# Optimization experiments

Measured on AMD Instinct MI355X. Metric: run time of the kernel, lower is better.

The kernel has to match this reference:

```python
import jax, jax.numpy as jnp
import numpy as np

EPS = 1e-6
NUM_HEADS = 16
ROPE_THETA = 100000.0


def _rope_tables(seq_len, head_dim, theta):
    inv_freq = 1.0 / (theta ** (np.arange(0, head_dim, 2, dtype=np.float32) / head_dim))
    t = np.arange(seq_len, dtype=np.float32)
    freqs = np.outer(t, inv_freq)                      # (S, head_dim//2)
    emb = np.concatenate([freqs, freqs], axis=-1)      # (S, head_dim)
    return jnp.asarray(np.cos(emb))[None], jnp.asarray(np.sin(emb))[None]  # (1,S,D)


def setup_inputs() -> dict:
    key = jax.random.key(0)
    ks = jax.random.split(key, 6)
    B, S, H = 2, 2048, 1024
    head_dim = H // NUM_HEADS
    cos, sin = _rope_tables(S, head_dim, ROPE_THETA)
    scale = 0.02
    return {
        "hidden_states": jax.random.normal(ks[0], (B, S, H), dtype=jnp.float32),
        "cos": cos, "sin": sin,
        "Wq": jax.random.normal(ks[1], (H, H), dtype=jnp.float32) * scale,
        "bq": jnp.zeros((H,), dtype=jnp.float32),
        "Wk": jax.random.normal(ks[2], (H, H), dtype=jnp.float32) * scale,
        "bk": jnp.zeros((H,), dtype=jnp.float32),
        "Wv": jax.random.normal(ks[3], (H, H), dtype=jnp.float32) * scale,
        "bv": jnp.zeros((H,), dtype=jnp.float32),
        "Wo": jax.random.normal(ks[4], (H, H), dtype=jnp.float32) * scale,
        "bo": jnp.zeros((H,), dtype=jnp.float32),
        "rms_weight": jnp.ones((H,), dtype=jnp.float32),
    }


def _rms_norm(x, w):
    var = jnp.mean(x * x, axis=-1, keepdims=True)
    return x * jax.lax.rsqrt(var + EPS) * w


def _rotate_half(x):
    x1, x2 = jnp.split(x, 2, axis=-1)
    return jnp.concatenate([-x2, x1], axis=-1)


def reference(hidden_states, cos, sin, Wq, bq, Wk, bk, Wv, bv, Wo, bo, rms_weight):
    B, S, H = hidden_states.shape
    D = H // NUM_HEADS
    q = hidden_states @ Wq.T + bq
    k = hidden_states @ Wk.T + bk
    v = hidden_states @ Wv.T + bv
    # RMSNorm over full hidden dim BEFORE head split (as in original)
    q = _rms_norm(q, rms_weight)
    k = _rms_norm(k, rms_weight)
    # (B,S,H) -> (B,heads,S,D)
    q = q.reshape(B, S, NUM_HEADS, D).transpose(0, 2, 1, 3)
    k = k.reshape(B, S, NUM_HEADS, D).transpose(0, 2, 1, 3)
    v = v.reshape(B, S, NUM_HEADS, D).transpose(0, 2, 1, 3)
    # RoPE: cos/sin (1,S,D) -> unsqueeze head dim
    c = cos[:, None, :, :]
    s = sin[:, None, :, :]
    q = q * c + _rotate_half(q) * s
    k = k * c + _rotate_half(k) * s
    # attention (faithful: boolean tril mask is ADDED as 0/1, not -inf)
    scale = D ** 0.5
    scores = jnp.einsum("bhqd,bhkd->bhqk", q, k) / scale
    mask = jnp.tril(jnp.ones((S, S), dtype=scores.dtype))  # +1 on causal, +0 elsewhere
    attn = jax.nn.softmax(scores + mask, axis=-1)
    out = jnp.einsum("bhqk,bhkd->bhqd", attn, v)
    out = out.transpose(0, 2, 1, 3).reshape(B, S, H)
    return out @ Wo.T + bo
```

## Files before the change

kernel.cpp:

```cpp
#include <hip/hip_runtime.h>

typedef unsigned short u16;
typedef __attribute__((ext_vector_type(8))) short bf16x8;
typedef __attribute__((ext_vector_type(4))) float f32x4;

#define MFMA16(A,B,C) __builtin_amdgcn_mfma_f32_16x16x32_bf16(A,B,C,0,0,0)
#define LOG2E 1.4426950408889634f
#define C1 0.18033688011112042f

__device__ __forceinline__ u16 f2bf(float f){
  unsigned int u; __builtin_memcpy(&u,&f,4);
  unsigned int r = (u + 0x7fffu + ((u>>16)&1u)) >> 16;
  return (u16)r;
}
__device__ __forceinline__ float bf2f(u16 h){
  unsigned int u = ((unsigned int)h) << 16;
  float f; __builtin_memcpy(&f,&u,4); return f;
}
__device__ __forceinline__ unsigned int pack_bf16(float a, float b){
  unsigned int ua, ub;
  __builtin_memcpy(&ua,&a,4); __builtin_memcpy(&ub,&b,4);
  ua = ua + 0x7fffu + ((ua>>16)&1u);
  ub = ub + 0x7fffu + ((ub>>16)&1u);
  return __builtin_amdgcn_perm(ub, ua, 0x07060302);
}

__device__ __forceinline__ void async_ld16(const void* g, void* l) {
  __builtin_amdgcn_global_load_lds(
      (const __attribute__((address_space(1))) unsigned int*)g,
      (__attribute__((address_space(3))) unsigned int*)l, 16, 0, 0);
}

__global__ __launch_bounds__(256) void cast_all(const float* __restrict__ hs,
    const float* __restrict__ wq, const float* __restrict__ wk,
    const float* __restrict__ wv, const float* __restrict__ wo,
    u16* __restrict__ dst)
{
  unsigned int i = blockIdx.x*256 + threadIdx.x;
  size_t el = (size_t)i * 8;
  const float* src; size_t off;
  if (el < 4194304) { src = hs; off = el; }
  else {
    unsigned int r = (unsigned int)((el - 4194304) >> 20);
    src = (r==0)?wq:(r==1)?wk:(r==2)?wv:wo;
    off = (el - 4194304) & 1048575;
  }
  float4 a = *reinterpret_cast<const float4*>(src+off);
  float4 b = *reinterpret_cast<const float4*>(src+off+4);
  u16 tmp[8] = {f2bf(a.x),f2bf(a.y),f2bf(a.z),f2bf(a.w),
                f2bf(b.x),f2bf(b.y),f2bf(b.z),f2bf(b.w)};
  *reinterpret_cast<uint4*>(dst + el) = *reinterpret_cast<const uint4*>(tmp);
}

__global__ __launch_bounds__(256) void gemm_qkv(const u16* __restrict__ A,
                                                const u16* __restrict__ W,
                                                const float* __restrict__ b0p,
                                                const float* __restrict__ b1p,
                                                const float* __restrict__ b2p,
                                                u16* __restrict__ out,
                                                int M, int N, int K)
{
  __shared__ __align__(16) u16 lds_a[128*32];
  __shared__ __align__(16) u16 lds_w[128*32];
  const int t = threadIdx.x;
  const int lane = t & 63, wave = t >> 6;
  const int wm = wave >> 1, wn = wave & 1;
  const int lr = lane & 15, quad = lane >> 4;
  const int n0 = blockIdx.x * 128, m0 = blockIdx.y * 128;
  const int wbase = t & 192;

  const f32x4 fzero = {0.f,0.f,0.f,0.f};
  f32x4 acc[4][4];
  #pragma unroll
  for (int i=0;i<4;++i)
    #pragma unroll
    for (int j=0;j<4;++j) acc[i][j] = fzero;

  for (int k0 = 0; k0 < K; k0 += 32) {
    __syncthreads();
    #pragma unroll
    for (int it=0; it<2; ++it) {
      int idx = it*256 + t;
      int row = idx >> 2, c8 = (idx & 3) * 8;
      int lbase = (it*256 + wbase) * 8;
      async_ld16(&A[(size_t)(m0+row)*K + k0 + c8], &lds_a[lbase]);
      async_ld16(&W[(size_t)(n0+row)*K + k0 + c8], &lds_w[lbase]);
    }
    __syncthreads();
    bf16x8 af[4], bfr[4];
    #pragma unroll
    for (int mt=0; mt<4; ++mt)
      af[mt] = *reinterpret_cast<const bf16x8*>(&lds_a[(wm*64 + mt*16 + lr)*32 + quad*8]);
    #pragma unroll
    for (int nt=0; nt<4; ++nt)
      bfr[nt] = *reinterpret_cast<const bf16x8*>(&lds_w[(wn*64 + nt*16 + lr)*32 + quad*8]);
    #pragma unroll
    for (int mt=0; mt<4; ++mt)
      #pragma unroll
      for (int nt=0; nt<4; ++nt)
        acc[mt][nt] = MFMA16(af[mt], bfr[nt], acc[mt][nt]);
  }

  int which = n0 >> 10;
  const float* bp = (which==0) ? b0p : (which==1) ? b1p : b2p;
  u16* dst = out + (size_t)which * 4194304;
  if (which == 2) {
    #pragma unroll
    for (int nt=0; nt<4; ++nt) {
      int nn = (n0 & 1023) + wn*64 + nt*16 + lr;
      float bv = bp[nn];
      int hh = nn >> 6, d = nn & 63;
      #pragma unroll
      for (int mt=0; mt<4; ++mt) {
        int m = m0 + wm*64 + mt*16 + quad*4;
        int b = m >> 11, s = m & 2047;
        u16 o[4];
        #pragma unroll
        for (int r=0; r<4; ++r) o[r] = f2bf(acc[mt][nt][r] + bv);
        *reinterpret_cast<uint2*>(&dst[((size_t)(b*16 + hh)*64 + d)*2048 + s]) =
            *reinterpret_cast<const uint2*>(o);
      }
    }
  } else {
    #pragma unroll
    for (int nt=0; nt<4; ++nt) {
      int nn = (n0 & 1023) + wn*64 + nt*16 + lr;
      float bv = bp[nn];
      int hh = nn >> 6, d = nn & 63;
      #pragma unroll
      for (int mt=0; mt<4; ++mt)
        #pragma unroll
        for (int r=0; r<4; ++r) {
          int m = m0 + wm*64 + mt*16 + quad*4 + r;
          int b = m >> 11, s = m & 2047;
          dst[((size_t)(b*16 + hh) * 2048 + s) * 64 + d] = f2bf(acc[mt][nt][r] + bv);
        }
    }
  }
}

__global__ __launch_bounds__(256) void gemm_o(const u16* __restrict__ A,
                                              const u16* __restrict__ W,
                                              const float* __restrict__ bias,
                                              float* __restrict__ O,
                                              int M, int N, int K)
{
  __shared__ __align__(16) u16 lds_a[128*32];
  __shared__ __align__(16) u16 lds_w[64*32];
  const int t = threadIdx.x;
  const int lane = t & 63, wm = t >> 6;
  const int lr = lane & 15, quad = lane >> 4;
  const int n0 = blockIdx.x * 64, m0 = blockIdx.y * 128;
  const int wbase = t & 192;

  const f32x4 fzero = {0.f,0.f,0.f,0.f};
  f32x4 acc[2][4];
  #pragma unroll
  for (int i=0;i<2;++i)
    #pragma unroll
    for (int j=0;j<4;++j) acc[i][j] = fzero;

  for (int k0 = 0; k0 < K; k0 += 32) {
    __syncthreads();
    #pragma unroll
    for (int it=0; it<2; ++it) {
      int idx = it*256 + t;
      int row = idx >> 2, c8 = (idx & 3) * 8;
      int lbase = (it*256 + wbase) * 8;
      async_ld16(&A[(size_t)(m0+row)*K + k0 + c8], &lds_a[lbase]);
    }
    async_ld16(&W[(size_t)(n0 + (t>>2))*K + k0 + (t&3)*8], &lds_w[wbase*8]);
    __syncthreads();
    bf16x8 af[2], bfr[4];
    #pragma unroll
    for (int mt=0; mt<2; ++mt)
      af[mt] = *reinterpret_cast<const bf16x8*>(&lds_a[(wm*32 + mt*16 + lr)*32 + quad*8]);
    #pragma unroll
    for (int nt=0; nt<4; ++nt)
      bfr[nt] = *reinterpret_cast<const bf16x8*>(&lds_w[(nt*16 + lr)*32 + quad*8]);
    #pragma unroll
    for (int mt=0; mt<2; ++mt)
      #pragma unroll
      for (int nt=0; nt<4; ++nt)
        acc[mt][nt] = MFMA16(af[mt], bfr[nt], acc[mt][nt]);
  }

  #pragma unroll
  for (int nt=0; nt<4; ++nt) {
    int n = n0 + nt*16 + lr;
    float bv = bias[n];
    #pragma unroll
    for (int mt=0; mt<2; ++mt)
      #pragma unroll
      for (int r=0; r<4; ++r) {
        int m = m0 + wm*32 + mt*16 + quad*4 + r;
        O[(size_t)m * N + n] = acc[mt][nt][r] + bv;
      }
  }
}

__global__ __launch_bounds__(256) void rmsrope(u16* __restrict__ qb, u16* __restrict__ kb,
                                               const float* __restrict__ cosb,
                                               const float* __restrict__ sinb,
                                               const float* __restrict__ w)
{
  u16* buf = blockIdx.y ? kb : qb;
  const int bs = blockIdx.x;
  const int b = bs >> 11, s = bs & 2047;
  const int t = threadIdx.x;
  float x1[2], x2[2];
  float ss = 0.f;
  #pragma unroll
  for (int i=0;i<2;++i){
    int p = t + i*256;
    int h = p >> 5, d = p & 31;
    size_t base = ((size_t)(b*16+h)*2048 + s)*64;
    x1[i] = bf2f(buf[base + d]);
    x2[i] = bf2f(buf[base + d + 32]);
    ss += x1[i]*x1[i] + x2[i]*x2[i];
  }
  #pragma unroll
  for (int off=32; off>0; off>>=1) ss += __shfl_xor(ss, off, 64);
  __shared__ float red[4];
  if ((t & 63) == 0) red[t>>6] = ss;
  __syncthreads();
  float tot = red[0]+red[1]+red[2]+red[3];
  float r = rsqrtf(tot * (1.0f/1024.0f) + 1e-6f);
  #pragma unroll
  for (int i=0;i<2;++i){
    int p = t + i*256;
    int h = p >> 5, d = p & 31;
    size_t base = ((size_t)(b*16+h)*2048 + s)*64;
    float w1 = w[h*64+d], w2 = w[h*64+d+32];
    float n1 = x1[i]*r*w1, n2 = x2[i]*r*w2;
    float c1 = cosb[s*64+d],    s1 = sinb[s*64+d];
    float c2 = cosb[s*64+d+32], s2 = sinb[s*64+d+32];
    buf[base+d]    = f2bf(n1*c1 - n2*s1);
    buf[base+d+32] = f2bf(n2*c2 + n1*s2);
  }
}

__global__ __launch_bounds__(256) void attn(const u16* __restrict__ qh,
                                            const u16* __restrict__ kh,
                                            const u16* __restrict__ vt,
                                            u16* __restrict__ ao)
{
  __shared__ __align__(16) u16 kbuf[64*72];
  __shared__ __align__(16) u16 vbuf[64*72];
  const int t = threadIdx.x;
  const int lane = t & 63, w = t >> 6;
  const int lr = lane & 15, quad = lane >> 4;
  const int bx = blockIdx.x;
  const int qbase = bx * 64;
  const int bh = blockIdx.y;
  const int b = bh >> 4, h = bh & 15;
  const size_t hb = (size_t)bh * 2048 * 64;
  const u16* qp = qh + hb;
  const u16* kp = kh + hb;
  const u16* vtp = vt + hb;

  const int q_abs = qbase + w*16 + lr;
  bf16x8 qf0 = *reinterpret_cast<const bf16x8*>(&qp[(size_t)q_abs*64 + quad*8]);
  bf16x8 qf1 = *reinterpret_cast<const bf16x8*>(&qp[(size_t)q_abs*64 + 32 + quad*8]);

  const int row0 = t >> 3;
  const int cc = t & 7;
  const int c8 = cc * 8;
  const int P0 = ((cc>>2)*32) + ((cc&1)*16) + (((cc>>1)&1)*4);
  u16* kw0 = &kbuf[row0*72 + c8];
  u16* kw1 = &kbuf[(row0+32)*72 + c8];
  u16* vw0 = &vbuf[row0*72 + P0];
  u16* vw1 = &vbuf[(row0+32)*72 + P0];

  const f32x4 fzero = {0.f,0.f,0.f,0.f};
  f32x4 oacc[4];
  #pragma unroll
  for (int i=0;i<4;++i) oacc[i] = fzero;
  float lsum = 0.f;
  const int qoff = w*16 + lr;

  for (int kt=0; kt<32; ++kt) {
    __syncthreads();
    {
      const u16* kg = kp + (size_t)kt*4096 + row0*64 + c8;
      const u16* vg = vtp + (size_t)row0*2048 + kt*64 + c8;
      uint4 k0 = *reinterpret_cast<const uint4*>(kg);
      uint4 k1 = *reinterpret_cast<const uint4*>(kg + 32*64);
      uint4 v0 = *reinterpret_cast<const uint4*>(vg);
      uint4 v1 = *reinterpret_cast<const uint4*>(vg + 32*2048);
      *reinterpret_cast<uint4*>(kw0) = k0;
      *reinterpret_cast<uint4*>(kw1) = k1;
      uint2 a0 = {v0.x, v0.y}, a1 = {v0.z, v0.w};
      uint2 b0 = {v1.x, v1.y}, b1 = {v1.z, v1.w};
      *reinterpret_cast<uint2*>(vw0)     = a0;
      *reinterpret_cast<uint2*>(vw0 + 8) = a1;
      *reinterpret_cast<uint2*>(vw1)     = b0;
      *reinterpret_cast<uint2*>(vw1 + 8) = b1;
    }
    __syncthreads();

    f32x4 zz[4];
    #pragma unroll
    for (int ksub=0; ksub<4; ++ksub) {
      const u16* kr = &kbuf[(ksub*16+lr)*72 + quad*8];
      bf16x8 a0, a1;
      __builtin_memcpy(&a0, kr, 16);
      __builtin_memcpy(&a1, kr+32, 16);
      f32x4 z = fzero;
      z = MFMA16(a0, qf0, z);
      z = MFMA16(a1, qf1, z);
      zz[ksub] = z;
    }

    unsigned int pk[4][2];
    if (kt != bx) {
      float ml = (kt < bx) ? LOG2E : 0.0f;
      #pragma unroll
      for (int ksub=0; ksub<4; ++ksub) {
        float p0 = __builtin_amdgcn_exp2f(__builtin_fmaf(zz[ksub][0], C1, ml));
        float p1 = __builtin_amdgcn_exp2f(__builtin_fmaf(zz[ksub][1], C1, ml));
        float p2 = __builtin_amdgcn_exp2f(__builtin_fmaf(zz[ksub][2], C1, ml));
        float p3 = __builtin_amdgcn_exp2f(__builtin_fmaf(zz[ksub][3], C1, ml));
        lsum += (p0+p1) + (p2+p3);
        pk[ksub][0] = pack_bf16(p0, p1);
        pk[ksub][1] = pack_bf16(p2, p3);
      }
    } else {
      #pragma unroll
      for (int ksub=0; ksub<4; ++ksub) {
        int koff = ksub*16 + quad*4;
        float p[4];
        #pragma unroll
        for (int r=0; r<4; ++r) {
          float ml = (koff + r <= qoff) ? LOG2E : 0.0f;
          p[r] = __builtin_amdgcn_exp2f(__builtin_fmaf(zz[ksub][r], C1, ml));
          lsum += p[r];
        }
        pk[ksub][0] = pack_bf16(p[0], p[1]);
        pk[ksub][1] = pack_bf16(p[2], p[3]);
      }
    }

    #pragma unroll
    for (int u=0; u<2; ++u) {
      uint4 pq = {pk[2*u][0], pk[2*u][1], pk[2*u+1][0], pk[2*u+1][1]};
      bf16x8 pf;
      __builtin_memcpy(&pf, &pq, 16);
      #pragma unroll
      for (int dt=0; dt<4; ++dt) {
        bf16x8 vf;
        __builtin_memcpy(&vf, &vbuf[(dt*16+lr)*72 + u*32 + quad*8], 16);
        oacc[dt] = MFMA16(vf, pf, oacc[dt]);
      }
    }
  }

  lsum += __shfl_xor(lsum, 16, 64);
  lsum += __shfl_xor(lsum, 32, 64);
  float inv = 1.0f / lsum;
  size_t rowbase = ((size_t)(b*2048 + q_abs))*1024 + h*64;
  #pragma unroll
  for (int dt=0; dt<4; ++dt) {
    u16 o[4];
    #pragma unroll
    for (int r=0; r<4; ++r) o[r] = f2bf(oacc[dt][r] * inv);
    *reinterpret_cast<uint2*>(&ao[rowbase + dt*16 + quad*4]) =
        *reinterpret_cast<const uint2*>(o);
  }
}

extern "C" void kernel_launch(void* const* d_in, const int* in_sizes, int n_in,
                              void* d_out, int out_size, void* d_ws, size_t ws_size,
                              hipStream_t stream)
{
  const float* hs   = (const float*)d_in[0];
  const float* cosb = (const float*)d_in[1];
  const float* sinb = (const float*)d_in[2];
  const float* Wq   = (const float*)d_in[3];
  const float* bq   = (const float*)d_in[4];
  const float* Wk   = (const float*)d_in[5];
  const float* bk   = (const float*)d_in[6];
  const float* Wv   = (const float*)d_in[7];
  const float* bv   = (const float*)d_in[8];
  const float* Wo   = (const float*)d_in[9];
  const float* bo   = (const float*)d_in[10];
  const float* rw   = (const float*)d_in[11];

  const size_t NEL = (size_t)4096 * 1024;
  const size_t WEL = (size_t)1024 * 1024;
  u16* hsb = (u16*)d_ws;
  u16* wqb = hsb + NEL;
  u16* wob = wqb + 3*WEL;
  u16* qhb = wob + WEL;
  u16* khb = qhb + NEL;
  u16* vtb = khb + NEL;
  u16* aob = hsb;

  cast_all<<<4096, 256, 0, stream>>>(hs, Wq, Wk, Wv, Wo, hsb);
  gemm_qkv<<<dim3(24,32), 256, 0, stream>>>(hsb, wqb, bq, bk, bv, qhb, 4096, 3072, 1024);
  rmsrope<<<dim3(4096,2), 256, 0, stream>>>(qhb, khb, cosb, sinb, rw);
  attn<<<dim3(32,32), 256, 0, stream>>>(qhb, khb, vtb, aob);
  gemm_o<<<dim3(16,32), 256, 0, stream>>>(aob, wob, bo, (float*)d_out, 4096, 1024, 1024);
}
```

Before: 235.2 us.

## Switch bf16 to fp16 throughout and widen attention blocks to 128 queries

Result: no change. 237.2 us (+0.8%).

```diff
diff --git a/kernel.cpp b/kernel.cpp
--- a/kernel.cpp
+++ b/kernel.cpp
@@ -1,28 +1,23 @@
 #include <hip/hip_runtime.h>
 
 typedef unsigned short u16;
-typedef __attribute__((ext_vector_type(8))) short bf16x8;
+typedef __attribute__((ext_vector_type(8))) _Float16 half8;
+typedef __attribute__((ext_vector_type(2))) __fp16 fp16x2;
 typedef __attribute__((ext_vector_type(4))) float f32x4;
 
-#define MFMA16(A,B,C) __builtin_amdgcn_mfma_f32_16x16x32_bf16(A,B,C,0,0,0)
+#define MFMAH(A,B,C) __builtin_amdgcn_mfma_f32_16x16x32_f16(A,B,C,0,0,0)
 #define LOG2E 1.4426950408889634f
 #define C1 0.18033688011112042f
 
-__device__ __forceinline__ u16 f2bf(float f){
-  unsigned int u; __builtin_memcpy(&u,&f,4);
-  unsigned int r = (u + 0x7fffu + ((u>>16)&1u)) >> 16;
-  return (u16)r;
-}
-__device__ __forceinline__ float bf2f(u16 h){
-  unsigned int u = ((unsigned int)h) << 16;
-  float f; __builtin_memcpy(&f,&u,4); return f;
-}
-__device__ __forceinline__ unsigned int pack_bf16(float a, float b){
-  unsigned int ua, ub;
-  __builtin_memcpy(&ua,&a,4); __builtin_memcpy(&ub,&b,4);
-  ua = ua + 0x7fffu + ((ua>>16)&1u);
-  ub = ub + 0x7fffu + ((ub>>16)&1u);
-  return __builtin_amdgcn_perm(ub, ua, 0x07060302);
+__device__ __forceinline__ u16 f2h(float f){
+  _Float16 h = (_Float16)f; u16 r; __builtin_memcpy(&r,&h,2); return r;
+}
+__device__ __forceinline__ float h2f(u16 v){
+  _Float16 h; __builtin_memcpy(&h,&v,2); return (float)h;
+}
+__device__ __forceinline__ unsigned int pack_h2(float a, float b){
+  fp16x2 h = __builtin_amdgcn_cvt_pkrtz(a,b);
+  unsigned int r; __builtin_memcpy(&r,&h,4); return r;
 }
 
 __device__ __forceinline__ void async_ld16(const void* g, void* l) {
@@ -47,9 +42,8 @@
   }
   float4 a = *reinterpret_cast<const float4*>(src+off);
   float4 b = *reinterpret_cast<const float4*>(src+off+4);
-  u16 tmp[8] = {f2bf(a.x),f2bf(a.y),f2bf(a.z),f2bf(a.w),
-                f2bf(b.x),f2bf(b.y),f2bf(b.z),f2bf(b.w)};
-  *reinterpret_cast<uint4*>(dst + el) = *reinterpret_cast<const uint4*>(tmp);
+  uint4 o = {pack_h2(a.x,a.y), pack_h2(a.z,a.w), pack_h2(b.x,b.y), pack_h2(b.z,b.w)};
+  *reinterpret_cast<uint4*>(dst + el) = o;
 }
 
 __global__ __launch_bounds__(256) void gemm_qkv(const u16* __restrict__ A,
@@ -87,18 +81,18 @@
       async_ld16(&W[(size_t)(n0+row)*K + k0 + c8], &lds_w[lbase]);
     }
     __syncthreads();
-    bf16x8 af[4], bfr[4];
+    half8 af[4], bfr[4];
     #pragma unroll
     for (int mt=0; mt<4; ++mt)
-      af[mt] = *reinterpret_cast<const bf16x8*>(&lds_a[(wm*64 + mt*16 + lr)*32 + quad*8]);
+      af[mt] = *reinterpret_cast<const half8*>(&lds_a[(wm*64 + mt*16 + lr)*32 + quad*8]);
     #pragma unroll
     for (int nt=0; nt<4; ++nt)
-      bfr[nt] = *reinterpret_cast<const bf16x8*>(&lds_w[(wn*64 + nt*16 + lr)*32 + quad*8]);
+      bfr[nt] = *reinterpret_cast<const half8*>(&lds_w[(wn*64 + nt*16 + lr)*32 + quad*8]);
     #pragma unroll
     for (int mt=0; mt<4; ++mt)
       #pragma unroll
       for (int nt=0; nt<4; ++nt)
-        acc[mt][nt] = MFMA16(af[mt], bfr[nt], acc[mt][nt]);
+        acc[mt][nt] = MFMAH(af[mt], bfr[nt], acc[mt][nt]);
   }
 
   int which = n0 >> 10;
@@ -114,11 +108,9 @@
       for (int mt=0; mt<4; ++mt) {
         int m = m0 + wm*64 + mt*16 + quad*4;
         int b = m >> 11, s = m & 2047;
-        u16 o[4];
-        #pragma unroll
-        for (int r=0; r<4; ++r) o[r] = f2bf(acc[mt][nt][r] + bv);
-        *reinterpret_cast<uint2*>(&dst[((size_t)(b*16 + hh)*64 + d)*2048 + s]) =
-            *reinterpret_cast<const uint2*>(o);
+        uint2 o = {pack_h2(acc[mt][nt][0]+bv, acc[mt][nt][1]+bv),
+                   pack_h2(acc[mt][nt][2]+bv, acc[mt][nt][3]+bv)};
+        *reinterpret_cast<uint2*>(&dst[((size_t)(b*16 + hh)*64 + d)*2048 + s]) = o;
       }
     }
   } else {
@@ -133,7 +125,7 @@
         for (int r=0; r<4; ++r) {
           int m = m0 + wm*64 + mt*16 + quad*4 + r;
           int b = m >> 11, s = m & 2047;
-          dst[((size_t)(b*16 + hh) * 2048 + s) * 64 + d] = f2bf(acc[mt][nt][r] + bv);
+          dst[((size_t)(b*16 + hh) * 2048 + s) * 64 + d] = f2h(acc[mt][nt][r] + bv);
         }
     }
   }
@@ -171,18 +163,18 @@
     }
     async_ld16(&W[(size_t)(n0 + (t>>2))*K + k0 + (t&3)*8], &lds_w[wbase*8]);
     __syncthreads();
-    bf16x8 af[2], bfr[4];
+    half8 af[2], bfr[4];
     #pragma unroll
     for (int mt=0; mt<2; ++mt)
-      af[mt] = *reinterpret_cast<const bf16x8*>(&lds_a[(wm*32 + mt*16 + lr)*32 + quad*8]);
+      af[mt] = *reinterpret_cast<const half8*>(&lds_a[(wm*32 + mt*16 + lr)*32 + quad*8]);
     #pragma unroll
     for (int nt=0; nt<4; ++nt)
-      bfr[nt] = *reinterpret_cast<const bf16x8*>(&lds_w[(nt*16 + lr)*32 + quad*8]);
+      bfr[nt] = *reinterpret_cast<const half8*>(&lds_w[(nt*16 + lr)*32 + quad*8]);
     #pragma unroll
     for (int mt=0; mt<2; ++mt)
       #pragma unroll
       for (int nt=0; nt<4; ++nt)
-        acc[mt][nt] = MFMA16(af[mt], bfr[nt], acc[mt][nt]);
+        acc[mt][nt] = MFMAH(af[mt], bfr[nt], acc[mt][nt]);
   }
 
   #pragma unroll
@@ -215,8 +207,8 @@
     int p = t + i*256;
     int h = p >> 5, d = p & 31;
     size_t base = ((size_t)(b*16+h)*2048 + s)*64;
-    x1[i] = bf2f(buf[base + d]);
-    x2[i] = bf2f(buf[base + d + 32]);
+    x1[i] = h2f(buf[base + d]);
+    x2[i] = h2f(buf[base + d + 32]);
     ss += x1[i]*x1[i] + x2[i]*x2[i];
   }
   #pragma unroll
@@ -235,12 +227,12 @@
     float n1 = x1[i]*r*w1, n2 = x2[i]*r*w2;
     float c1 = cosb[s*64+d],    s1 = sinb[s*64+d];
     float c2 = cosb[s*64+d+32], s2 = sinb[s*64+d+32];
-    buf[base+d]    = f2bf(n1*c1 - n2*s1);
-    buf[base+d+32] = f2bf(n2*c2 + n1*s2);
-  }
-}
-
-__global__ __launch_bounds__(256) void attn(const u16* __restrict__ qh,
+    buf[base+d]    = f2h(n1*c1 - n2*s1);
+    buf[base+d+32] = f2h(n2*c2 + n1*s2);
+  }
+}
+
+__global__ __launch_bounds__(512) void attn(const u16* __restrict__ qh,
                                             const u16* __restrict__ kh,
                                             const u16* __restrict__ vt,
                                             u16* __restrict__ ao)
@@ -251,7 +243,7 @@
   const int lane = t & 63, w = t >> 6;
   const int lr = lane & 15, quad = lane >> 4;
   const int bx = blockIdx.x;
-  const int qbase = bx * 64;
+  const int qbase = bx * 128;
   const int bh = blockIdx.y;
   const int b = bh >> 4, h = bh & 15;
   const size_t hb = (size_t)bh * 2048 * 64;
@@ -260,42 +252,34 @@
   const u16* vtp = vt + hb;
 
   const int q_abs = qbase + w*16 + lr;
-  bf16x8 qf0 = *reinterpret_cast<const bf16x8*>(&qp[(size_t)q_abs*64 + quad*8]);
-  bf16x8 qf1 = *reinterpret_cast<const bf16x8*>(&qp[(size_t)q_abs*64 + 32 + quad*8]);
-
-  const int row0 = t >> 3;
+  half8 qf0 = *reinterpret_cast<const half8*>(&qp[(size_t)q_abs*64 + quad*8]);
+  half8 qf1 = *reinterpret_cast<const half8*>(&qp[(size_t)q_abs*64 + 32 + quad*8]);
+
+  const int row = t >> 3;
   const int cc = t & 7;
-  const int c8 = cc * 8;
-  const int P0 = ((cc>>2)*32) + ((cc&1)*16) + (((cc>>1)&1)*4);
-  u16* kw0 = &kbuf[row0*72 + c8];
-  u16* kw1 = &kbuf[(row0+32)*72 + c8];
-  u16* vw0 = &vbuf[row0*72 + P0];
-  u16* vw1 = &vbuf[(row0+32)*72 + P0];
+  const int vu = cc >> 2, vq = cc & 3;
+  const int k1 = vu*32 + vq*4;
+  u16* kw = &kbuf[row*72 + cc*8];
+  u16* vw = &vbuf[row*72 + cc*8];
+  const u16* kg = kp + (size_t)row*64 + cc*8;
+  const u16* vg = vtp + (size_t)row*2048 + k1;
 
   const f32x4 fzero = {0.f,0.f,0.f,0.f};
   f32x4 oacc[4];
   #pragma unroll
   for (int i=0;i<4;++i) oacc[i] = fzero;
   float lsum = 0.f;
-  const int qoff = w*16 + lr;
+  const int diag = (qbase + w*16) >> 6;
 
   for (int kt=0; kt<32; ++kt) {
     __syncthreads();
     {
-      const u16* kg = kp + (size_t)kt*4096 + row0*64 + c8;
-      const u16* vg = vtp + (size_t)row0*2048 + kt*64 + c8;
-      uint4 k0 = *reinterpret_cast<const uint4*>(kg);
-      uint4 k1 = *reinterpret_cast<const uint4*>(kg + 32*64);
-      uint4 v0 = *reinterpret_cast<const uint4*>(vg);
-      uint4 v1 = *reinterpret_cast<const uint4*>(vg + 32*2048);
-      *reinterpret_cast<uint4*>(kw0) = k0;
-      *reinterpret_cast<uint4*>(kw1) = k1;
-      uint2 a0 = {v0.x, v0.y}, a1 = {v0.z, v0.w};
-      uint2 b0 = {v1.x, v1.y}, b1 = {v1.z, v1.w};
-      *reinterpret_cast<uint2*>(vw0)     = a0;
-      *reinterpret_cast<uint2*>(vw0 + 8) = a1;
-      *reinterpret_cast<uint2*>(vw1)     = b0;
-      *reinterpret_cast<uint2*>(vw1 + 8) = b1;
+      uint4 kv = *reinterpret_cast<const uint4*>(kg + (size_t)kt*4096);
+      uint2 g1 = *reinterpret_cast<const uint2*>(vg + kt*64);
+      uint2 g2 = *reinterpret_cast<const uint2*>(vg + kt*64 + 16);
+      *reinterpret_cast<uint4*>(kw) = kv;
+      uint4 vv = {g1.x, g1.y, g2.x, g2.y};
+      *reinterpret_cast<uint4*>(vw) = vv;
     }
     __syncthreads();
 
@@ -303,18 +287,18 @@
     #pragma unroll
     for (int ksub=0; ksub<4; ++ksub) {
       const u16* kr = &kbuf[(ksub*16+lr)*72 + quad*8];
-      bf16x8 a0, a1;
+      half8 a0, a1;
       __builtin_memcpy(&a0, kr, 16);
       __builtin_memcpy(&a1, kr+32, 16);
       f32x4 z = fzero;
-      z = MFMA16(a0, qf0, z);
-      z = MFMA16(a1, qf1, z);
+      z = MFMAH(a0, qf0, z);
+      z = MFMAH(a1, qf1, z);
       zz[ksub] = z;
     }
 
     unsigned int pk[4][2];
-    if (kt != bx) {
-      float ml = (kt < bx) ? LOG2E : 0.0f;
+    if (kt != diag) {
+      float ml = (kt < diag) ? LOG2E : 0.0f;
       #pragma unroll
       for (int ksub=0; ksub<4; ++ksub) {
         float p0 = __builtin_amdgcn_exp2f(__builtin_fmaf(zz[ksub][0], C1, ml));
@@ -322,35 +306,35 @@
         float p2 = __builtin_amdgcn_exp2f(__builtin_fmaf(zz[ksub][2], C1, ml));
         float p3 = __builtin_amdgcn_exp2f(__builtin_fmaf(zz[ksub][3], C1, ml));
         lsum += (p0+p1) + (p2+p3);
-        pk[ksub][0] = pack_bf16(p0, p1);
-        pk[ksub][1] = pack_bf16(p2, p3);
+        pk[ksub][0] = pack_h2(p0, p1);
+        pk[ksub][1] = pack_h2(p2, p3);
       }
     } else {
       #pragma unroll
       for (int ksub=0; ksub<4; ++ksub) {
-        int koff = ksub*16 + quad*4;
+        int key0 = kt*64 + ksub*16 + quad*4;
         float p[4];
         #pragma unroll
         for (int r=0; r<4; ++r) {
-          float ml = (koff + r <= qoff) ? LOG2E : 0.0f;
+          float ml = (key0 + r <= q_abs) ? LOG2E : 0.0f;
           p[r] = __builtin_amdgcn_exp2f(__builtin_fmaf(zz[ksub][r], C1, ml));
           lsum += p[r];
         }
-        pk[ksub][0] = pack_bf16(p[0], p[1]);
-        pk[ksub][1] = pack_bf16(p[2], p[3]);
+        pk[ksub][0] = pack_h2(p[0], p[1]);
+        pk[ksub][1] = pack_h2(p[2], p[3]);
       }
     }
 
     #pragma unroll
     for (int u=0; u<2; ++u) {
       uint4 pq = {pk[2*u][0], pk[2*u][1], pk[2*u+1][0], pk[2*u+1][1]};
-      bf16x8 pf;
+      half8 pf;
       __builtin_memcpy(&pf, &pq, 16);
       #pragma unroll
       for (int dt=0; dt<4; ++dt) {
-        bf16x8 vf;
+        half8 vf;
         __builtin_memcpy(&vf, &vbuf[(dt*16+lr)*72 + u*32 + quad*8], 16);
-        oacc[dt] = MFMA16(vf, pf, oacc[dt]);
+        oacc[dt] = MFMAH(vf, pf, oacc[dt]);
       }
     }
   }
@@ -361,11 +345,9 @@
   size_t rowbase = ((size_t)(b*2048 + q_abs))*1024 + h*64;
   #pragma unroll
   for (int dt=0; dt<4; ++dt) {
-    u16 o[4];
-    #pragma unroll
-    for (int r=0; r<4; ++r) o[r] = f2bf(oacc[dt][r] * inv);
-    *reinterpret_cast<uint2*>(&ao[rowbase + dt*16 + quad*4]) =
-        *reinterpret_cast<const uint2*>(o);
+    uint2 o = {pack_h2(oacc[dt][0]*inv, oacc[dt][1]*inv),
+               pack_h2(oacc[dt][2]*inv, oacc[dt][3]*inv)};
+    *reinterpret_cast<uint2*>(&ao[rowbase + dt*16 + quad*4]) = o;
   }
 }
 
@@ -399,6 +381,6 @@
   cast_all<<<4096, 256, 0, stream>>>(hs, Wq, Wk, Wv, Wo, hsb);
   gemm_qkv<<<dim3(24,32), 256, 0, stream>>>(hsb, wqb, bq, bk, bv, qhb, 4096, 3072, 1024);
   rmsrope<<<dim3(4096,2), 256, 0, stream>>>(qhb, khb, cosb, sinb, rw);
-  attn<<<dim3(32,32), 256, 0, stream>>>(qhb, khb, vtb, aob);
+  attn<<<dim3(16,32), 512, 0, stream>>>(qhb, khb, vtb, aob);
   gemm_o<<<dim3(16,32), 256, 0, stream>>>(aob, wob, bo, (float*)d_out, 4096, 1024, 1024);
 }
```
